# Kernel tuning notes

Measured on AMD Instinct MI355X. Metric: run time of the kernel, lower is better.

Reference implementation:

```python
import jax, jax.numpy as jnp
import numpy as np

DIM = 64        # feature size per vector
CODES = 512     # codebook size (called d_model in the torch module)
DECAY = 0.99
EPS = 1e-5


def setup_inputs() -> dict:
    key = jax.random.key(0)
    k1, k2 = jax.random.split(key)
    x = jax.random.normal(k1, (64, 64, 64, 64), dtype=jnp.float32)
    embedding = jax.random.normal(k2, (DIM, CODES), dtype=jnp.float32)
    N = jnp.zeros((CODES,), dtype=jnp.float32)
    M = embedding.copy()  # torch module initializes M as embedding.clone()
    return {"x": x, "embedding": embedding, "N": N, "M": M}


def reference(x, embedding, N, M):
    # flatten tokens: [T, DIM]
    flatten = x.reshape(-1, DIM)
    # squared L2 distance to every code: [T, CODES]
    distance = (jnp.sum(flatten * flatten, axis=1, keepdims=True)
                - 2.0 * flatten @ embedding
                + jnp.sum(embedding * embedding, axis=0, keepdims=True))
    max_index = jnp.argmin(distance, axis=1)          # (-distance).max(1) == argmin
    indices = max_index.reshape(x.shape[:-1])
    # gather codes: embedding.T is [CODES, DIM]
    quantize = jnp.take(embedding.T, max_index, axis=0).reshape(x.shape)

    # EMA codebook update (training=True). Avoid materializing onehot:
    # ni = onehot.sum(0); eofx = flatten.T @ onehot  -> segment sums over codes.
    ni = jax.ops.segment_sum(jnp.ones_like(max_index, dtype=jnp.float32),
                             max_index, num_segments=CODES)          # [CODES]
    eofx = jax.ops.segment_sum(flatten, max_index, num_segments=CODES).T  # [DIM, CODES]
    N_new = N * DECAY + (1.0 - DECAY) * ni
    M_new = M * DECAY + (1.0 - DECAY) * eofx
    n = jnp.sum(N_new)
    N_smoothed = (N_new + EPS) / (n + CODES * EPS) * n
    embedding_new = M_new / N_smoothed

    quant_loss = jnp.mean((jax.lax.stop_gradient(x) - quantize) ** 2)
    commitment_loss = jnp.mean((jax.lax.stop_gradient(quantize) - x) ** 2)
    quantize_st = x + jax.lax.stop_gradient(quantize - x)  # straight-through
    return (quantize_st, quant_loss, indices, commitment_loss,
            embedding_new, N_new, M_new)
```

## Files before the change

kernel.cpp:

```cpp
#include <hip/hip_runtime.h>
#include <hip/hip_bf16.h>
#include <math.h>

#define DIM 64
#define CODES 512
#define TOKENS 262144
#define XELEMS 16777216

#define DECAYF 0.99f
#define OMDECAY 0.01f
#define EPSF 1e-5f

#define WS_CNORM 0
#define WS_NI    512
#define WS_EOFX  1024
#define WS_LOSS  33792
#define WS_ET    33808
#define WS_IMG   66576
#define WS_PART  99344
#define PART_STRIDE 33280
#define NPART 256

#define OFF_Q    0
#define OFF_QL   16777216
#define OFF_IDX  16777217
#define OFF_CL   17039361
#define OFF_ENEW 17039362
#define OFF_NNEW 17072130
#define OFF_MNEW 17072642

typedef __attribute__((ext_vector_type(8))) short bf16x8;
typedef __attribute__((ext_vector_type(4))) float f32x4;

static __device__ inline void split_bf(float v, short& hi, short& lo) {
  unsigned int b = __float_as_uint(v);
  unsigned int hb = b & 0xffff0000u;
  float lof = v - __uint_as_float(hb);
  hi = (short)(b >> 16);
  lo = (short)(__float_as_uint(lof) >> 16);
}

__global__ __launch_bounds__(256) void vq_prep(const float* __restrict__ emb,
                                               float* __restrict__ ws) {
  int c = blockIdx.x * 256 + threadIdx.x;
  unsigned short* img = (unsigned short*)(ws + WS_IMG);
  float* eT = ws + WS_ET;
  int cc = c >> 4;
  int n = c & 15;
  float cn = 0.f;
#pragma unroll
  for (int d0 = 0; d0 < DIM; d0 += 4) {
    float v[4];
#pragma unroll
    for (int u = 0; u < 4; ++u) {
      v[u] = emb[(d0 + u) * CODES + c];
      cn = fmaf(v[u], v[u], cn);
    }
    *(float4*)(eT + (size_t)c * DIM + d0) = make_float4(v[0], v[1], v[2], v[3]);
    int kh = d0 >> 5, kk = d0 & 31, qd = kk >> 3, j0 = kk & 7;
    int lane = qd * 16 + n;
    short hi[4], lo[4];
#pragma unroll
    for (int u = 0; u < 4; ++u) split_bf(v[u], hi[u], lo[u]);
    int base = cc * 2048 + kh * 1024 + lane * 8 + j0;
    *(ushort4*)(img + base) =
        make_ushort4((unsigned short)hi[0], (unsigned short)hi[1],
                     (unsigned short)hi[2], (unsigned short)hi[3]);
    *(ushort4*)(img + base + 512) =
        make_ushort4((unsigned short)lo[0], (unsigned short)lo[1],
                     (unsigned short)lo[2], (unsigned short)lo[3]);
  }
  ws[WS_CNORM + c] = cn;
}

__global__ __launch_bounds__(256, 4) void vq_screen(
    const float* __restrict__ x, const float* __restrict__ ws,
    float* __restrict__ loss_sum, float* __restrict__ q_out,
    float* __restrict__ idx_out) {
  __shared__ float cn_l[CODES];

  const float* eT = ws + WS_ET;
  const unsigned short* gimg = (const unsigned short*)(ws + WS_IMG);

  for (int i = threadIdx.x; i < CODES; i += 256) cn_l[i] = ws[WS_CNORM + i];
  __syncthreads();

  const int lane = threadIdx.x & 63;
  const int wave = threadIdx.x >> 6;
  const int n = lane & 15;
  const int quad = lane >> 4;
  const int t0 = blockIdx.x * 256 + wave * 64;

  const float INITP = __uint_as_float((__float_as_uint(1e30f) & 0xFFFFFE00u) | 511u);
  float loss = 0.f;

#pragma unroll 1
  for (int pair = 0; pair < 2; ++pair) {
    bf16x8 ah[2][2], al[2][2];
#pragma unroll
    for (int tile = 0; tile < 2; ++tile) {
      const float* xr =
          x + (size_t)(t0 + (pair * 2 + tile) * 16 + n) * DIM + quad * 8;
#pragma unroll
      for (int kh = 0; kh < 2; ++kh) {
        float4 va = *(const float4*)(xr + kh * 32);
        float4 vb = *(const float4*)(xr + kh * 32 + 4);
        float f[8] = {va.x, va.y, va.z, va.w, vb.x, vb.y, vb.z, vb.w};
#pragma unroll
        for (int j = 0; j < 8; ++j) {
          short hi, lo;
          split_bf(-2.f * f[j], hi, lo);
          ah[tile][kh][j] = hi;
          al[tile][kh][j] = lo;
        }
      }
    }

    float v1[2][4], v2[2][4];
#pragma unroll
    for (int tile = 0; tile < 2; ++tile)
#pragma unroll
      for (int r = 0; r < 4; ++r) {
        v1[tile][r] = INITP;
        v2[tile][r] = INITP;
      }

    bf16x8 Pa0, Pa1, Pa2, Pa3, Pb0, Pb1, Pb2, Pb3;
    {
      const unsigned short* bq = gimg + lane * 8;
      Pa0 = *(const bf16x8*)(bq);
      Pa1 = *(const bf16x8*)(bq + 512);
      Pa2 = *(const bf16x8*)(bq + 1024);
      Pa3 = *(const bf16x8*)(bq + 1536);
    }

    auto ccbody = [&](int cc, const bf16x8& ch0, const bf16x8& cl0,
                      const bf16x8& ch1, const bf16x8& cl1, bf16x8& nh0,
                      bf16x8& nl0, bf16x8& nh1, bf16x8& nl1) {
      const unsigned short* bq = gimg + ((cc + 1) & 31) * 2048 + lane * 8;
      nh0 = *(const bf16x8*)(bq);
      nl0 = *(const bf16x8*)(bq + 512);
      nh1 = *(const bf16x8*)(bq + 1024);
      nl1 = *(const bf16x8*)(bq + 1536);
      float cnv = cn_l[cc * 16 + n];
      unsigned int cid = (unsigned int)(cc * 16 + n);
#pragma unroll
      for (int tile = 0; tile < 2; ++tile) {
        f32x4 acc = {0.f, 0.f, 0.f, 0.f};
        acc = __builtin_amdgcn_mfma_f32_16x16x32_bf16(ah[tile][0], ch0, acc, 0, 0, 0);
        acc = __builtin_amdgcn_mfma_f32_16x16x32_bf16(al[tile][0], ch0, acc, 0, 0, 0);
        acc = __builtin_amdgcn_mfma_f32_16x16x32_bf16(ah[tile][0], cl0, acc, 0, 0, 0);
        acc = __builtin_amdgcn_mfma_f32_16x16x32_bf16(ah[tile][1], ch1, acc, 0, 0, 0);
        acc = __builtin_amdgcn_mfma_f32_16x16x32_bf16(al[tile][1], ch1, acc, 0, 0, 0);
        acc = __builtin_amdgcn_mfma_f32_16x16x32_bf16(ah[tile][1], cl1, acc, 0, 0, 0);
#pragma unroll
        for (int r = 0; r < 4; ++r) {
          float s = acc[r] + cnv;
          float sp = __uint_as_float((__float_as_uint(s) & 0xFFFFFE00u) | cid);
          float o1 = v1[tile][r];
          v2[tile][r] = __builtin_amdgcn_fmed3f(sp, o1, v2[tile][r]);
          v1[tile][r] = fminf(sp, o1);
        }
      }
    };

    for (int cc = 0; cc < 32; cc += 2) {
      ccbody(cc, Pa0, Pa1, Pa2, Pa3, Pb0, Pb1, Pb2, Pb3);
      ccbody(cc + 1, Pb0, Pb1, Pb2, Pb3, Pa0, Pa1, Pa2, Pa3);
    }

#pragma unroll
    for (int m = 1; m < 16; m <<= 1) {
#pragma unroll
      for (int tile = 0; tile < 2; ++tile)
#pragma unroll
        for (int r = 0; r < 4; ++r) {
          float o1 = __shfl_xor(v1[tile][r], m, 16);
          float o2 = __shfl_xor(v2[tile][r], m, 16);
          float a = v1[tile][r];
          v1[tile][r] = fminf(a, o1);
          v2[tile][r] = fminf(fminf(v2[tile][r], o2), fmaxf(a, o1));
        }
    }

#pragma unroll
    for (int tile = 0; tile < 2; ++tile) {
      int tt = pair * 2 + tile;
#pragma unroll
      for (int r = 0; r < 4; ++r) {
        int t = t0 + tt * 16 + quad * 4 + r;
        int c1 = (int)(__float_as_uint(v1[tile][r]) & 511u);
        int c2 = (int)(__float_as_uint(v2[tile][r]) & 511u);
        float4 xv = *(const float4*)(x + (size_t)t * DIM + n * 4);
        float4 e1 = *(const float4*)(eT + (size_t)c1 * DIM + n * 4);
        float4 e2 = *(const float4*)(eT + (size_t)c2 * DIM + n * 4);
        float p1 = xv.x * e1.x;
        p1 = fmaf(xv.y, e1.y, p1);
        p1 = fmaf(xv.z, e1.z, p1);
        p1 = fmaf(xv.w, e1.w, p1);
        float p2 = xv.x * e2.x;
        p2 = fmaf(xv.y, e2.y, p2);
        p2 = fmaf(xv.z, e2.z, p2);
        p2 = fmaf(xv.w, e2.w, p2);
#pragma unroll
        for (int m = 1; m < 16; m <<= 1) {
          p1 += __shfl_xor(p1, m, 16);
          p2 += __shfl_xor(p2, m, 16);
        }
        float d1 = fmaf(-2.f, p1, cn_l[c1]);
        float d2 = fmaf(-2.f, p2, cn_l[c2]);
        bool take2 = (d2 < d1) || (d2 == d1 && c2 < c1);
        int w = take2 ? c2 : c1;
        float4 q = take2 ? e2 : e1;
        *(float4*)(q_out + (size_t)t * DIM + n * 4) = q;
        float u0 = xv.x - q.x, u1 = xv.y - q.y;
        float u2 = xv.z - q.z, u3 = xv.w - q.w;
        loss = fmaf(u0, u0, loss);
        loss = fmaf(u1, u1, loss);
        loss = fmaf(u2, u2, loss);
        loss = fmaf(u3, u3, loss);
        if (n == 0) idx_out[t] = (float)w;
      }
    }
  }

#pragma unroll
  for (int off = 32; off > 0; off >>= 1) loss += __shfl_down(loss, off, 64);
  if (lane == 0) atomicAdd(loss_sum, loss);
}

__global__ __launch_bounds__(1024, 1) void vq_scatter(
    const float* __restrict__ x, const float* __restrict__ idx_out,
    float* __restrict__ part_base, int aflush, float* __restrict__ ws_acc) {
  __shared__ __align__(16) unsigned char smem[71808];
  float* lds_e = (float*)smem;
  float* lds_n = (float*)(smem + 65664);
  int* win_l = (int*)(smem + 67712);

  const int lane = threadIdx.x & 63;
  const int wave = threadIdx.x >> 6;
  const int n = lane & 15;
  const int quad = lane >> 4;
  const int t0 = blockIdx.x * 1024 + wave * 64;

  {
    float4 z = make_float4(0.f, 0.f, 0.f, 0.f);
    float4* zp = (float4*)smem;
    for (int i = threadIdx.x; i < 67712 / 16; i += 1024) zp[i] = z;
  }
  win_l[threadIdx.x] = (int)idx_out[blockIdx.x * 1024 + threadIdx.x];
  __syncthreads();

#pragma unroll 1
  for (int kh = 0; kh < 2; ++kh) {
#pragma unroll
    for (int tile = 0; tile < 4; ++tile) {
      int wbi = win_l[wave * 64 + tile * 16 + n];
      if (kh == 0 && quad == 0) atomicAdd(&lds_n[wbi], 1.0f);
      const float* xr =
          x + (size_t)(t0 + tile * 16 + n) * DIM + kh * 32 + quad * 8;
      float4 xa = *(const float4*)(xr);
      float4 xb = *(const float4*)(xr + 4);
      int k0 = quad * 8;
      atomicAdd(&lds_e[(k0 + 0) * 513 + wbi], xa.x);
      atomicAdd(&lds_e[(k0 + 1) * 513 + wbi], xa.y);
      atomicAdd(&lds_e[(k0 + 2) * 513 + wbi], xa.z);
      atomicAdd(&lds_e[(k0 + 3) * 513 + wbi], xa.w);
      atomicAdd(&lds_e[(k0 + 4) * 513 + wbi], xb.x);
      atomicAdd(&lds_e[(k0 + 5) * 513 + wbi], xb.y);
      atomicAdd(&lds_e[(k0 + 6) * 513 + wbi], xb.z);
      atomicAdd(&lds_e[(k0 + 7) * 513 + wbi], xb.w);
    }
    __syncthreads();
    if (aflush) {
      if (kh == 0) {
        for (int i = threadIdx.x; i < CODES; i += 1024) {
          float v = lds_n[i];
          if (v != 0.f) atomicAdd(&ws_acc[WS_NI + i], v);
        }
      }
      for (int i = threadIdx.x; i < 32 * CODES; i += 1024) {
        int k = i >> 9, c = i & 511;
        float v = lds_e[k * 513 + c];
        if (v != 0.f) atomicAdd(&ws_acc[WS_EOFX + kh * 32 * CODES + i], v);
        if (kh == 0) lds_e[k * 513 + c] = 0.f;
      }
    } else {
      float* dest = part_base + (size_t)blockIdx.x * PART_STRIDE;
      if (kh == 0) {
        for (int i = threadIdx.x; i < CODES; i += 1024) dest[i] = lds_n[i];
      }
      for (int i = threadIdx.x; i < 32 * CODES; i += 1024) {
        int k = i >> 9, c = i & 511;
        dest[CODES + kh * 32 * CODES + i] = lds_e[k * 513 + c];
        if (kh == 0) lds_e[k * 513 + c] = 0.f;
      }
    }
    if (kh == 0) __syncthreads();
  }
}

__global__ __launch_bounds__(256) void vq_reduce(const float* __restrict__ part,
                                                 float* __restrict__ ws, int P) {
  int i = blockIdx.x * 256 + threadIdx.x;
  if (i >= PART_STRIDE) return;
  int cp = P >> 3;
  int p0 = blockIdx.y * cp;
  int pe = p0 + cp;
  float a0 = 0.f, a1 = 0.f, a2 = 0.f, a3 = 0.f;
  int p = p0;
  for (; p + 3 < pe; p += 4) {
    a0 += part[(size_t)(p + 0) * PART_STRIDE + i];
    a1 += part[(size_t)(p + 1) * PART_STRIDE + i];
    a2 += part[(size_t)(p + 2) * PART_STRIDE + i];
    a3 += part[(size_t)(p + 3) * PART_STRIDE + i];
  }
  for (; p < pe; ++p) a0 += part[(size_t)p * PART_STRIDE + i];
  atomicAdd(&ws[WS_NI + i], (a0 + a1) + (a2 + a3));
}

__global__ __launch_bounds__(512) void vq_final(const float* __restrict__ Nin,
                                                const float* __restrict__ Min,
                                                const float* __restrict__ ws,
                                                float* __restrict__ out) {
  __shared__ float red[512];
  int c = threadIdx.x;
  int d = blockIdx.x;
  float niv = ws[WS_NI + c];
  float Nn = Nin[c] * DECAYF + OMDECAY * niv;
  red[c] = Nn;
  __syncthreads();
#pragma unroll
  for (int s = 256; s > 0; s >>= 1) {
    if (c < s) red[c] += red[c + s];
    __syncthreads();
  }
  float nsum = red[0];
  float Nsm = (Nn + EPSF) / (nsum + (float)CODES * EPSF) * nsum;
  float m = Min[d * CODES + c] * DECAYF + OMDECAY * ws[WS_EOFX + d * CODES + c];
  out[OFF_MNEW + d * CODES + c] = m;
  out[OFF_ENEW + d * CODES + c] = m / Nsm;
  if (d == 0) {
    out[OFF_NNEW + c] = Nn;
    if (c == 0) {
      float l = ws[WS_LOSS] / (float)XELEMS;
      out[OFF_QL] = l;
      out[OFF_CL] = l;
    }
  }
}

extern "C" void kernel_launch(void* const* d_in, const int* in_sizes, int n_in,
                              void* d_out, int out_size, void* d_ws, size_t ws_size,
                              hipStream_t stream) {
  const float* x = (const float*)d_in[0];
  const float* emb = (const float*)d_in[1];
  const float* Nin = (const float*)d_in[2];
  const float* Min = (const float*)d_in[3];
  float* out = (float*)d_out;
  float* ws = (float*)d_ws;

  size_t avail = ws_size / 4;
  int aflush = (avail < (size_t)WS_PART + (size_t)NPART * PART_STRIDE) ? 1 : 0;

  hipMemsetAsync(ws + WS_NI, 0, (size_t)(WS_ET - WS_NI) * sizeof(float), stream);

  vq_prep<<<2, 256, 0, stream>>>(emb, ws);

  vq_screen<<<TOKENS / 256, 256, 0, stream>>>(x, ws, ws + WS_LOSS, out + OFF_Q,
                                              out + OFF_IDX);

  vq_scatter<<<TOKENS / 1024, 1024, 0, stream>>>(x, out + OFF_IDX, ws + WS_PART,
                                                 aflush, ws);

  if (!aflush) {
    vq_reduce<<<dim3((PART_STRIDE + 255) / 256, 8), 256, 0, stream>>>(
        ws + WS_PART, ws, NPART);
  }

  vq_final<<<DIM, 512, 0, stream>>>(Nin, Min, ws, out);
}
```

Measured before the change: 319.5 us.

## Flush scatter partials with global atomics and drop separate reduce kernel

The scatter kernel always pushes its per-block LDS histograms and code sums straight to global memory with atomic adds, instead of writing 256 full partial buffers and launching a separate reduction kernel. Each block starts its flush at a different offset (eight rotations by block index) so concurrent blocks hit different addresses and contend less on the same atomics. This drops about 34 MB of partial-buffer writes and reads plus one kernel launch. In exchange it adds heavy global atomic traffic, and the float sums now depend on the order the atomics land.

After: 323.6 us. No clear change (+1.3%).

```diff
diff --git a/kernel.cpp b/kernel.cpp
--- a/kernel.cpp
+++ b/kernel.cpp
@@ -17,9 +17,6 @@
 #define WS_LOSS  33792
 #define WS_ET    33808
 #define WS_IMG   66576
-#define WS_PART  99344
-#define PART_STRIDE 33280
-#define NPART 256
 
 #define OFF_Q    0
 #define OFF_QL   16777216
@@ -231,7 +228,7 @@
 
 __global__ __launch_bounds__(1024, 1) void vq_scatter(
     const float* __restrict__ x, const float* __restrict__ idx_out,
-    float* __restrict__ part_base, int aflush, float* __restrict__ ws_acc) {
+    float* __restrict__ ws_acc) {
   __shared__ __align__(16) unsigned char smem[71808];
   float* lds_e = (float*)smem;
   float* lds_n = (float*)(smem + 65664);
@@ -250,6 +247,9 @@
   }
   win_l[threadIdx.x] = (int)idx_out[blockIdx.x * 1024 + threadIdx.x];
   __syncthreads();
+
+  const int rotE = (blockIdx.x & 7) * 2048;
+  const int rotN = (blockIdx.x & 7) * 64;
 
 #pragma unroll 1
   for (int kh = 0; kh < 2; ++kh) {
@@ -272,51 +272,22 @@
       atomicAdd(&lds_e[(k0 + 7) * 513 + wbi], xb.w);
     }
     __syncthreads();
-    if (aflush) {
-      if (kh == 0) {
-        for (int i = threadIdx.x; i < CODES; i += 1024) {
-          float v = lds_n[i];
-          if (v != 0.f) atomicAdd(&ws_acc[WS_NI + i], v);
-        }
-      }
-      for (int i = threadIdx.x; i < 32 * CODES; i += 1024) {
-        int k = i >> 9, c = i & 511;
-        float v = lds_e[k * 513 + c];
-        if (v != 0.f) atomicAdd(&ws_acc[WS_EOFX + kh * 32 * CODES + i], v);
-        if (kh == 0) lds_e[k * 513 + c] = 0.f;
-      }
-    } else {
-      float* dest = part_base + (size_t)blockIdx.x * PART_STRIDE;
-      if (kh == 0) {
-        for (int i = threadIdx.x; i < CODES; i += 1024) dest[i] = lds_n[i];
-      }
-      for (int i = threadIdx.x; i < 32 * CODES; i += 1024) {
-        int k = i >> 9, c = i & 511;
-        dest[CODES + kh * 32 * CODES + i] = lds_e[k * 513 + c];
-        if (kh == 0) lds_e[k * 513 + c] = 0.f;
-      }
+    if (kh == 0) {
+      for (int ii = threadIdx.x; ii < CODES; ii += 1024) {
+        int i = (ii + rotN) & (CODES - 1);
+        float v = lds_n[i];
+        if (v != 0.f) atomicAdd(&ws_acc[WS_NI + i], v);
+      }
+    }
+    for (int ii = threadIdx.x; ii < 32 * CODES; ii += 1024) {
+      int i = (ii + rotE) & (32 * CODES - 1);
+      int k = i >> 9, c = i & 511;
+      float v = lds_e[k * 513 + c];
+      if (v != 0.f) atomicAdd(&ws_acc[WS_EOFX + kh * 32 * CODES + i], v);
+      if (kh == 0) lds_e[k * 513 + c] = 0.f;
     }
     if (kh == 0) __syncthreads();
   }
-}
-
-__global__ __launch_bounds__(256) void vq_reduce(const float* __restrict__ part,
-                                                 float* __restrict__ ws, int P) {
-  int i = blockIdx.x * 256 + threadIdx.x;
-  if (i >= PART_STRIDE) return;
-  int cp = P >> 3;
-  int p0 = blockIdx.y * cp;
-  int pe = p0 + cp;
-  float a0 = 0.f, a1 = 0.f, a2 = 0.f, a3 = 0.f;
-  int p = p0;
-  for (; p + 3 < pe; p += 4) {
-    a0 += part[(size_t)(p + 0) * PART_STRIDE + i];
-    a1 += part[(size_t)(p + 1) * PART_STRIDE + i];
-    a2 += part[(size_t)(p + 2) * PART_STRIDE + i];
-    a3 += part[(size_t)(p + 3) * PART_STRIDE + i];
-  }
-  for (; p < pe; ++p) a0 += part[(size_t)p * PART_STRIDE + i];
-  atomicAdd(&ws[WS_NI + i], (a0 + a1) + (a2 + a3));
 }
 
 __global__ __launch_bounds__(512) void vq_final(const float* __restrict__ Nin,
@@ -360,9 +331,6 @@
   float* out = (float*)d_out;
   float* ws = (float*)d_ws;
 
-  size_t avail = ws_size / 4;
-  int aflush = (avail < (size_t)WS_PART + (size_t)NPART * PART_STRIDE) ? 1 : 0;
-
   hipMemsetAsync(ws + WS_NI, 0, (size_t)(WS_ET - WS_NI) * sizeof(float), stream);
 
   vq_prep<<<2, 256, 0, stream>>>(emb, ws);
@@ -370,13 +338,7 @@
   vq_screen<<<TOKENS / 256, 256, 0, stream>>>(x, ws, ws + WS_LOSS, out + OFF_Q,
                                               out + OFF_IDX);
 
-  vq_scatter<<<TOKENS / 1024, 1024, 0, stream>>>(x, out + OFF_IDX, ws + WS_PART,
-                                                 aflush, ws);
-
-  if (!aflush) {
-    vq_reduce<<<dim3((PART_STRIDE + 255) / 256, 8), 256, 0, stream>>>(
-        ws + WS_PART, ws, NPART);
-  }
+  vq_scatter<<<TOKENS / 1024, 1024, 0, stream>>>(x, out + OFF_IDX, ws);
 
   vq_final<<<DIM, 512, 0, stream>>>(Nin, Min, ws, out);
 }
```
